# Kernel tuning notes

Hardware: AMD Instinct MI355X
Metric: run time of the kernel (lower is better)

Reference implementation:

```python
import jax, jax.numpy as jnp
import numpy as np

MODEL_DIM = 256
PAIR_IMPORTANCE_WEIGHT = 0.5
B, S, D = 4, 4096, MODEL_DIM


def setup_inputs() -> dict:
    key = jax.random.key(0)
    ks = jax.random.split(key, 6)
    return {
        "query": jax.random.normal(ks[0], (B, S, D), dtype=jnp.float32),
        "key": jax.random.normal(ks[1], (B, S, D), dtype=jnp.float32),
        "value": jax.random.normal(ks[2], (B, S, D), dtype=jnp.float32),
        "W_query": jax.random.normal(ks[3], (D, D), dtype=jnp.float32),
        "W_key": jax.random.normal(ks[4], (D, D), dtype=jnp.float32),
        "W_value": jax.random.normal(ks[5], (D, D), dtype=jnp.float32),
    }


def reference(query, key, value, W_query, W_key, W_value):
    # Projections: [B,S,D] @ [D,D]
    q = jnp.einsum('bsd,de->bse', query, W_query)
    k = jnp.einsum('bsd,de->bse', key, W_key)
    v = jnp.einsum('bsd,de->bse', value, W_value)
    scale = jnp.sqrt(jnp.asarray(MODEL_DIM, dtype=q.dtype))
    # Full [B,S,S] score matrix (global max forces materialization)
    scores = jnp.einsum('bqd,bkd->bqk', q, k) / scale
    s_len = scores.shape[1]
    diag_bias = jnp.eye(s_len, dtype=scores.dtype) * jnp.max(scores)
    scores = scores + PAIR_IMPORTANCE_WEIGHT * diag_bias  # broadcast over batch
    attention_weights = jax.nn.softmax(scores, axis=-1)
    output = jnp.einsum('bqk,bkd->bqd', attention_weights, v)
    return output, attention_weights
```

## Files before the change

### kernel.cpp

```cpp
#include <hip/hip_runtime.h>
#include <cstdint>
#include <cstddef>

#define BB 4
#define SS 4096
#define DD 256
#define SCORE_SCALE (1.0f/16.0f)
#define PIW 0.5f
#define NROWS (BB * SS)

typedef float          f32x4  __attribute__((ext_vector_type(4)));
typedef __bf16         bf16v8 __attribute__((ext_vector_type(8)));
typedef unsigned short u16v8  __attribute__((ext_vector_type(8)));
typedef unsigned short u16v4  __attribute__((ext_vector_type(4)));

__device__ __forceinline__ f32x4 mfma_bf16(u16v8 a, u16v8 b, f32x4 c) {
    return __builtin_amdgcn_mfma_f32_16x16x32_bf16(
        __builtin_bit_cast(bf16v8, a), __builtin_bit_cast(bf16v8, b), c, 0, 0, 0);
}

__device__ __forceinline__ unsigned short f2bf(float f) {
    unsigned u = __float_as_uint(f);
    u += 0x7FFFu + ((u >> 16) & 1u);
    return (unsigned short)(u >> 16);
}
__device__ __forceinline__ float bf2f(unsigned short h) {
    return __uint_as_float(((unsigned)h) << 16);
}
__device__ __forceinline__ unsigned fenc(float x) {
    unsigned u = __float_as_uint(x);
    return (u & 0x80000000u) ? ~u : (u | 0x80000000u);
}
__device__ __forceinline__ float fdec(unsigned e) {
    return __uint_as_float((e & 0x80000000u) ? (e ^ 0x80000000u) : ~e);
}

#define TM 128
#define TN 128
#define TK 16
#define PADW 132

__global__ __launch_bounds__(256) void proj_kernel(
    const float* __restrict__ query, const float* __restrict__ key_, const float* __restrict__ value,
    const float* __restrict__ Wq, const float* __restrict__ Wk, const float* __restrict__ Wv,
    unsigned short* __restrict__ qh, unsigned short* __restrict__ ql,
    unsigned short* __restrict__ kh, unsigned short* __restrict__ kl,
    unsigned short* __restrict__ vT, unsigned* __restrict__ gmax)
{
    const int z = blockIdx.z;
    const float* A = (z == 0) ? query : (z == 1) ? key_ : value;
    const float* W = (z == 0) ? Wq    : (z == 1) ? Wk   : Wv;
    if (z == 0 && blockIdx.x == 0 && blockIdx.y == 0 && threadIdx.x == 0)
        *gmax = 0x007FFFFFu;

    const int K = DD, N = DD;
    __shared__ float As[TK][PADW];
    __shared__ float Bs[TK][PADW];
    const int tid = threadIdx.x;
    const int tx = tid & 15, ty = tid >> 4;
    const int rowBase = blockIdx.y * TM;
    const int colBase = blockIdx.x * TN;

    float acc[8][8] = {};

    for (int k0 = 0; k0 < K; k0 += TK) {
        #pragma unroll
        for (int i = 0; i < 2; i++) {
            int idx = tid + i * 256;
            int r = idx >> 2, kq = idx & 3;
            const float4 av = *(const float4*)&A[(size_t)(rowBase + r) * K + k0 + kq * 4];
            As[kq * 4 + 0][r] = av.x; As[kq * 4 + 1][r] = av.y;
            As[kq * 4 + 2][r] = av.z; As[kq * 4 + 3][r] = av.w;
        }
        #pragma unroll
        for (int i = 0; i < 2; i++) {
            int idx = tid + i * 256;
            int kk = idx >> 5, cq = idx & 31;
            *(float4*)&Bs[kk][cq * 4] = *(const float4*)&W[(size_t)(k0 + kk) * N + colBase + cq * 4];
        }
        __syncthreads();
        #pragma unroll
        for (int kk = 0; kk < TK; kk++) {
            float a[8], b[8];
            *(float4*)&a[0] = *(const float4*)&As[kk][ty * 8];
            *(float4*)&a[4] = *(const float4*)&As[kk][ty * 8 + 4];
            *(float4*)&b[0] = *(const float4*)&Bs[kk][tx * 8];
            *(float4*)&b[4] = *(const float4*)&Bs[kk][tx * 8 + 4];
            #pragma unroll
            for (int i = 0; i < 8; i++)
                #pragma unroll
                for (int j = 0; j < 8; j++)
                    acc[i][j] = fmaf(a[i], b[j], acc[i][j]);
        }
        __syncthreads();
    }

    #pragma unroll
    for (int i = 0; i < 8; i++) {
        const int gr = rowBase + ty * 8 + i;
        if (z == 2) {
            const int b2 = gr >> 12, s2 = gr & (SS - 1);
            #pragma unroll
            for (int j = 0; j < 8; j++) {
                int col = colBase + tx * 8 + j;
                vT[((size_t)b2 * DD + col) * SS + s2] = f2bf(acc[i][j]);
            }
        } else {
            unsigned short h[8], l[8];
            #pragma unroll
            for (int j = 0; j < 8; j++) {
                h[j] = f2bf(acc[i][j]);
                l[j] = f2bf(acc[i][j] - bf2f(h[j]));
            }
            unsigned short* H = (z == 0) ? qh : kh;
            unsigned short* L = (z == 0) ? ql : kl;
            size_t base = (size_t)gr * DD + colBase + tx * 8;
            *(u16v4*)&H[base]     = (u16v4){h[0], h[1], h[2], h[3]};
            *(u16v4*)&H[base + 4] = (u16v4){h[4], h[5], h[6], h[7]};
            *(u16v4*)&L[base]     = (u16v4){l[0], l[1], l[2], l[3]};
            *(u16v4*)&L[base + 4] = (u16v4){l[4], l[5], l[6], l[7]};
        }
    }
}

#define SPAD 40

__global__ __launch_bounds__(256) void scores_mfma(
    const unsigned short* __restrict__ qh, const unsigned short* __restrict__ ql,
    const unsigned short* __restrict__ kh, const unsigned short* __restrict__ kl,
    float* __restrict__ attn, unsigned* __restrict__ gmax,
    float* __restrict__ tmaxg, float* __restrict__ tsumg)
{
    const int b = blockIdx.z;
    const size_t boff = (size_t)b * SS * DD;
    const unsigned short* Qh = qh + boff;
    const unsigned short* Ql = ql + boff;
    const unsigned short* Kh = kh + boff;
    const unsigned short* Kl = kl + boff;
    float* C = attn + (size_t)b * SS * SS;

    __shared__ unsigned short Ah[128][SPAD];
    __shared__ unsigned short Al[128][SPAD];
    __shared__ unsigned short Bh[128][SPAD];
    __shared__ unsigned short Bl[128][SPAD];
    __shared__ float s_m[4][64];
    __shared__ float s_s[4][64];
    __shared__ float red[128];

    const int tid = threadIdx.x;
    const int lane = tid & 63, w = tid >> 6;
    const int wr = (w >> 1) * 64, wc = (w & 1) * 64;
    const int m = lane & 15, qq = lane >> 4;
    const int rowBase = blockIdx.y * 128;
    const int colBase = blockIdx.x * 128;

    f32x4 acc[4][4];
    #pragma unroll
    for (int i = 0; i < 4; i++)
        #pragma unroll
        for (int j = 0; j < 4; j++)
            acc[i][j] = (f32x4){0.f, 0.f, 0.f, 0.f};

    const int chunk = (tid & 3) * 8;
    const int srow  = tid >> 2;

    for (int k0 = 0; k0 < DD; k0 += 32) {
        #pragma unroll
        for (int i = 0; i < 2; i++) {
            int r = srow + i * 64;
            size_t ga = (size_t)(rowBase + r) * DD + k0 + chunk;
            size_t gb = (size_t)(colBase + r) * DD + k0 + chunk;
            *(u16v8*)&Ah[r][chunk] = *(const u16v8*)&Qh[ga];
            *(u16v8*)&Al[r][chunk] = *(const u16v8*)&Ql[ga];
            *(u16v8*)&Bh[r][chunk] = *(const u16v8*)&Kh[gb];
            *(u16v8*)&Bl[r][chunk] = *(const u16v8*)&Kl[gb];
        }
        __syncthreads();

        const int kb = qq * 8;
        u16v8 ah[4], al[4], bh[4], bl[4];
        #pragma unroll
        for (int i = 0; i < 4; i++) {
            ah[i] = *(const u16v8*)&Ah[wr + i * 16 + m][kb];
            al[i] = *(const u16v8*)&Al[wr + i * 16 + m][kb];
            bh[i] = *(const u16v8*)&Bh[wc + i * 16 + m][kb];
            bl[i] = *(const u16v8*)&Bl[wc + i * 16 + m][kb];
        }
        #pragma unroll
        for (int i = 0; i < 4; i++)
            #pragma unroll
            for (int j = 0; j < 4; j++) {
                acc[i][j] = mfma_bf16(ah[i], bh[j], acc[i][j]);
                acc[i][j] = mfma_bf16(ah[i], bl[j], acc[i][j]);
                acc[i][j] = mfma_bf16(al[i], bh[j], acc[i][j]);
            }
        __syncthreads();
    }

    #pragma unroll
    for (int i = 0; i < 4; i++)
        #pragma unroll
        for (int j = 0; j < 4; j++)
            acc[i][j] *= SCORE_SCALE;

    #pragma unroll
    for (int i = 0; i < 4; i++)
        #pragma unroll
        for (int j = 0; j < 4; j++)
            #pragma unroll
            for (int r = 0; r < 4; r++) {
                int row = rowBase + wr + i * 16 + qq * 4 + r;
                int col = colBase + wc + j * 16 + m;
                __builtin_nontemporal_store(acc[i][j][r], &C[(size_t)row * SS + col]);
            }

    float lmax[16];
    #pragma unroll
    for (int i = 0; i < 4; i++)
        #pragma unroll
        for (int r = 0; r < 4; r++)
            lmax[i * 4 + r] = fmaxf(fmaxf(acc[i][0][r], acc[i][1][r]),
                                    fmaxf(acc[i][2][r], acc[i][3][r]));
    #pragma unroll
    for (int t = 0; t < 16; t++) {
        #pragma unroll
        for (int msk = 1; msk < 16; msk <<= 1)
            lmax[t] = fmaxf(lmax[t], __shfl_xor(lmax[t], msk));
    }
    if (m == 0) {
        #pragma unroll
        for (int i = 0; i < 4; i++)
            #pragma unroll
            for (int r = 0; r < 4; r++)
                s_m[w][i * 16 + qq * 4 + r] = lmax[i * 4 + r];
    }
    __syncthreads();
    float lsum[16];
    #pragma unroll
    for (int i = 0; i < 4; i++)
        #pragma unroll
        for (int r = 0; r < 4; r++) {
            int idx = i * 16 + qq * 4 + r;
            float rm = fmaxf(s_m[w][idx], s_m[w ^ 1][idx]);
            float s = 0.f;
            #pragma unroll
            for (int j = 0; j < 4; j++)
                s += __expf(acc[i][j][r] - rm);
            lsum[i * 4 + r] = s;
        }
    #pragma unroll
    for (int t = 0; t < 16; t++) {
        #pragma unroll
        for (int msk = 1; msk < 16; msk <<= 1)
            lsum[t] += __shfl_xor(lsum[t], msk);
    }
    if (m == 0) {
        #pragma unroll
        for (int i = 0; i < 4; i++)
            #pragma unroll
            for (int r = 0; r < 4; r++)
                s_s[w][i * 16 + qq * 4 + r] = lsum[i * 4 + r];
    }
    __syncthreads();

    if (tid < 128) {
        int wp = tid >> 6, lr = tid & 63;
        float tm = fmaxf(s_m[2 * wp][lr], s_m[2 * wp + 1][lr]);
        float ts = s_s[2 * wp][lr] + s_s[2 * wp + 1][lr];
        size_t gi = (size_t)blockIdx.x * NROWS + (size_t)b * SS + rowBase + tid;
        tmaxg[gi] = tm;
        tsumg[gi] = ts;
        red[tid] = tm;
    }
    __syncthreads();
    for (int s2 = 64; s2 > 0; s2 >>= 1) {
        if (tid < s2) red[tid] = fmaxf(red[tid], red[tid + s2]);
        __syncthreads();
    }
    if (tid == 0) atomicMax(gmax, fenc(red[0]));
}

__global__ __launch_bounds__(256) void stats_merge(
    const float* __restrict__ tmaxg, const float* __restrict__ tsumg,
    const float* __restrict__ attn, const unsigned* __restrict__ gmax,
    float* __restrict__ rowm, float* __restrict__ rowinv)
{
    const int grow = blockIdx.x * 256 + threadIdx.x;
    const int b = grow >> 12, i = grow & (SS - 1);
    const float bias = PIW * fdec(*gmax);

    float tm[32];
    float mx = -INFINITY;
    #pragma unroll
    for (int t = 0; t < 32; t++) {
        tm[t] = tmaxg[(size_t)t * NROWS + grow];
        mx = fmaxf(mx, tm[t]);
    }
    const float dii = attn[(size_t)b * SS * SS + (size_t)i * SS + i];
    mx = fmaxf(mx, dii + bias);

    float s = 0.f;
    #pragma unroll
    for (int t = 0; t < 32; t++)
        s += tsumg[(size_t)t * NROWS + grow] * __expf(tm[t] - mx);
    s += __expf(dii + bias - mx) - __expf(dii - mx);

    rowm[grow] = mx;
    rowinv[grow] = 1.0f / s;
}

__global__ __launch_bounds__(256) void av_softmax_mfma(
    float* __restrict__ attn, const unsigned short* __restrict__ vT,
    const float* __restrict__ rowm, const float* __restrict__ rowinv,
    const unsigned* __restrict__ gmax, float* __restrict__ out)
{
    const int lin = blockIdx.x;
    const int b = (lin & 7) >> 1;
    const int rowTile = ((lin >> 3) << 1) | (lin & 1);
    const int rowBase = rowTile * 32;

    float* A = attn + (size_t)b * SS * SS;
    const unsigned short* Bv = vT + (size_t)b * DD * SS;
    const float bias = PIW * fdec(*gmax);

    __shared__ unsigned short As[2][32][136];

    const int tid = threadIdx.x;
    const int lane = tid & 63, w = tid >> 6;
    const int m = lane & 15, qq = lane >> 4;

    const int ra = tid >> 3;
    const int c0 = (tid & 7) * 4;
    const int rr = rowBase + ra;
    float* Arow = A + (size_t)rr * SS;
    const float mr = rowm[b * SS + rr];
    const float ri = rowinv[b * SS + rr];

    const unsigned short* Bp[4];
    #pragma unroll
    for (int j = 0; j < 4; j++)
        Bp[j] = Bv + (size_t)(w * 64 + j * 16 + m) * SS;

    f32x4 acc[2][4];
    #pragma unroll
    for (int i = 0; i < 2; i++)
        #pragma unroll
        for (int j = 0; j < 4; j++)
            acc[i][j] = (f32x4){0.f, 0.f, 0.f, 0.f};

    f32x4 pf[4];

    auto loadA = [&](int kbase) {
        #pragma unroll
        for (int u = 0; u < 4; u++)
            pf[u] = __builtin_nontemporal_load(
                (const f32x4*)&Arow[kbase + c0 + u * 32]);
    };
    auto procStore = [&](int kbase, int buf) {
        #pragma unroll
        for (int u = 0; u < 4; u++) {
            int c = c0 + u * 32;
            int j0 = kbase + c;
            float e0 = pf[u][0] + ((j0 + 0 == rr) ? bias : 0.0f);
            float e1 = pf[u][1] + ((j0 + 1 == rr) ? bias : 0.0f);
            float e2 = pf[u][2] + ((j0 + 2 == rr) ? bias : 0.0f);
            float e3 = pf[u][3] + ((j0 + 3 == rr) ? bias : 0.0f);
            float w0 = __expf(e0 - mr) * ri;
            float w1 = __expf(e1 - mr) * ri;
            float w2 = __expf(e2 - mr) * ri;
            float w3 = __expf(e3 - mr) * ri;
            f32x4 wv = (f32x4){w0, w1, w2, w3};
            __builtin_nontemporal_store(wv, (f32x4*)&Arow[j0]);
            *(u16v4*)&As[buf][ra][c] =
                (u16v4){f2bf(w0), f2bf(w1), f2bf(w2), f2bf(w3)};
        }
    };

    const int NT = SS / 128;

    loadA(0);
    procStore(0, 0);
    __syncthreads();

    for (int t = 0; t < NT; t++) {
        const int k0 = t * 128;
        const int cur = t & 1;
        if (t + 1 < NT)
            loadA(k0 + 128);
        #pragma unroll
        for (int kk = 0; kk < 4; kk++) {
            const int kb = kk * 32 + qq * 8;
            u16v8 bf_[4], af_[2];
            #pragma unroll
            for (int j = 0; j < 4; j++)
                bf_[j] = *(const u16v8*)&Bp[j][k0 + kb];
            #pragma unroll
            for (int i = 0; i < 2; i++)
                af_[i] = *(const u16v8*)&As[cur][i * 16 + m][kb];
            #pragma unroll
            for (int i = 0; i < 2; i++)
                #pragma unroll
                for (int j = 0; j < 4; j++)
                    acc[i][j] = mfma_bf16(af_[i], bf_[j], acc[i][j]);
        }
        if (t + 1 < NT) {
            procStore(k0 + 128, cur ^ 1);
            __syncthreads();
        }
    }

    #pragma unroll
    for (int i = 0; i < 2; i++) {
        #pragma unroll
        for (int j = 0; j < 4; j++) {
            #pragma unroll
            for (int r = 0; r < 4; r++) {
                int row = rowBase + i * 16 + qq * 4 + r;
                int col = w * 64 + j * 16 + m;
                __builtin_nontemporal_store(
                    acc[i][j][r], &out[((size_t)b * SS + row) * DD + col]);
            }
        }
    }
}

extern "C" void kernel_launch(void* const* d_in, const int* in_sizes, int n_in,
                              void* d_out, int out_size, void* d_ws, size_t ws_size,
                              hipStream_t stream)
{
    const float* query = (const float*)d_in[0];
    const float* key_  = (const float*)d_in[1];
    const float* value = (const float*)d_in[2];
    const float* Wq    = (const float*)d_in[3];
    const float* Wk    = (const float*)d_in[4];
    const float* Wv    = (const float*)d_in[5];

    float* out  = (float*)d_out;
    float* attn = out + (size_t)BB * SS * DD;

    const size_t E = (size_t)BB * SS * DD;
    unsigned short* qh = (unsigned short*)d_ws;
    unsigned short* ql = qh + E;
    unsigned short* kh = ql + E;
    unsigned short* kl = kh + E;
    unsigned short* vT = kl + E;
    float* tmaxg  = (float*)(vT + E);
    float* tsumg  = tmaxg + 32 * (size_t)NROWS;
    float* rowm   = tsumg + 32 * (size_t)NROWS;
    float* rowinv = rowm + NROWS;
    unsigned* gmax = (unsigned*)(rowinv + NROWS);

    proj_kernel<<<dim3(DD / TN, (BB * SS) / TM, 3), 256, 0, stream>>>(
        query, key_, value, Wq, Wk, Wv, qh, ql, kh, kl, vT, gmax);
    scores_mfma<<<dim3(SS / 128, SS / 128, BB), 256, 0, stream>>>(
        qh, ql, kh, kl, attn, gmax, tmaxg, tsumg);
    stats_merge<<<dim3(NROWS / 256), 256, 0, stream>>>(
        tmaxg, tsumg, attn, gmax, rowm, rowinv);
    av_softmax_mfma<<<dim3(512), 256, 0, stream>>>(
        attn, vT, rowm, rowinv, gmax, out);
}
```

Measured before the change: 672.7 us.

## Restructure AV softmax kernel to register-resident A fragments with split-K reduction

Reworks the attention-weights-times-V kernel so each lane loads its own score fragment directly in MFMA A-operand layout, applies bias, exp and normalization in registers, and feeds it straight to the MFMA. This removes the shared-memory staging buffer and the per-tile __syncthreads. Each wave now computes all 256 output columns for 16 rows over half the key dimension. Wave pairs then combine their partial accumulators through LDS at the end. The price is a much larger register footprint (16 accumulators, 16 B fragments, two prefetch buffers), which may lower occupancy, plus more redundant V loads per wave.

```diff
diff --git a/kernel.cpp b/kernel.cpp
--- a/kernel.cpp
+++ b/kernel.cpp
@@ -309,6 +309,41 @@
     rowinv[grow] = 1.0f / s;
 }
 
+#define AV_LOADA(pf, lk)                                                      \
+    _Pragma("unroll")                                                         \
+    for (int v_ = 0; v_ < 4; v_++) {                                          \
+        pf[2*v_]   = __builtin_nontemporal_load(                              \
+            (const f32x4*)&Arow[(lk) + v_*32 + qq*8]);                        \
+        pf[2*v_+1] = __builtin_nontemporal_load(                              \
+            (const f32x4*)&Arow[(lk) + v_*32 + qq*8 + 4]);                    \
+    }
+
+#define AV_KK(pf, kkk, lk)                                                    \
+    {                                                                         \
+        const int cb_ = (lk) + (kkk)*32 + qq*8;                               \
+        _Pragma("unroll")                                                     \
+        for (int n_ = 0; n_ < 16; n_++)                                       \
+            bf[n_] = *(const u16v8*)&Bp[n_][cb_];                             \
+        f32x4 lo_ = pf[2*(kkk)], hi_ = pf[2*(kkk)+1];                         \
+        float wv_[8];                                                         \
+        _Pragma("unroll")                                                     \
+        for (int e_ = 0; e_ < 8; e_++) {                                      \
+            float x_ = (e_ < 4) ? lo_[e_ & 3] : hi_[e_ & 3];                  \
+            x_ += ((cg0 + cb_ + e_) == rr) ? bias : 0.0f;                     \
+            wv_[e_] = __expf(x_ - mr) * ri;                                   \
+        }                                                                     \
+        __builtin_nontemporal_store((f32x4){wv_[0], wv_[1], wv_[2], wv_[3]},  \
+                                    (f32x4*)&Arow[cb_]);                      \
+        __builtin_nontemporal_store((f32x4){wv_[4], wv_[5], wv_[6], wv_[7]},  \
+                                    (f32x4*)&Arow[cb_ + 4]);                  \
+        u16v8 af_ = (u16v8){f2bf(wv_[0]), f2bf(wv_[1]), f2bf(wv_[2]),         \
+                            f2bf(wv_[3]), f2bf(wv_[4]), f2bf(wv_[5]),         \
+                            f2bf(wv_[6]), f2bf(wv_[7])};                      \
+        _Pragma("unroll")                                                     \
+        for (int n_ = 0; n_ < 16; n_++)                                       \
+            acc[n_] = mfma_bf16(af_, bf[n_], acc[n_]);                        \
+    }
+
 __global__ __launch_bounds__(256) void av_softmax_mfma(
     float* __restrict__ attn, const unsigned short* __restrict__ vT,
     const float* __restrict__ rowm, const float* __restrict__ rowinv,
@@ -323,102 +358,68 @@
     const unsigned short* Bv = vT + (size_t)b * DD * SS;
     const float bias = PIW * fdec(*gmax);
 
-    __shared__ unsigned short As[2][32][136];
+    __shared__ float redl[2][64][64];
 
     const int tid = threadIdx.x;
     const int lane = tid & 63, w = tid >> 6;
+    const int pair = w >> 1;
+    const int u = w & 1;
     const int m = lane & 15, qq = lane >> 4;
 
-    const int ra = tid >> 3;
-    const int c0 = (tid & 7) * 4;
-    const int rr = rowBase + ra;
-    float* Arow = A + (size_t)rr * SS;
+    const int rr = rowBase + pair * 16 + m;
+    const int cg0 = u * 2048;
+    float* Arow = A + (size_t)rr * SS + cg0;
     const float mr = rowm[b * SS + rr];
     const float ri = rowinv[b * SS + rr];
 
-    const unsigned short* Bp[4];
-    #pragma unroll
-    for (int j = 0; j < 4; j++)
-        Bp[j] = Bv + (size_t)(w * 64 + j * 16 + m) * SS;
-
-    f32x4 acc[2][4];
-    #pragma unroll
-    for (int i = 0; i < 2; i++)
-        #pragma unroll
-        for (int j = 0; j < 4; j++)
-            acc[i][j] = (f32x4){0.f, 0.f, 0.f, 0.f};
-
-    f32x4 pf[4];
-
-    auto loadA = [&](int kbase) {
-        #pragma unroll
-        for (int u = 0; u < 4; u++)
-            pf[u] = __builtin_nontemporal_load(
-                (const f32x4*)&Arow[kbase + c0 + u * 32]);
-    };
-    auto procStore = [&](int kbase, int buf) {
-        #pragma unroll
-        for (int u = 0; u < 4; u++) {
-            int c = c0 + u * 32;
-            int j0 = kbase + c;
-            float e0 = pf[u][0] + ((j0 + 0 == rr) ? bias : 0.0f);
-            float e1 = pf[u][1] + ((j0 + 1 == rr) ? bias : 0.0f);
-            float e2 = pf[u][2] + ((j0 + 2 == rr) ? bias : 0.0f);
-            float e3 = pf[u][3] + ((j0 + 3 == rr) ? bias : 0.0f);
-            float w0 = __expf(e0 - mr) * ri;
-            float w1 = __expf(e1 - mr) * ri;
-            float w2 = __expf(e2 - mr) * ri;
-            float w3 = __expf(e3 - mr) * ri;
-            f32x4 wv = (f32x4){w0, w1, w2, w3};
-            __builtin_nontemporal_store(wv, (f32x4*)&Arow[j0]);
-            *(u16v4*)&As[buf][ra][c] =
-                (u16v4){f2bf(w0), f2bf(w1), f2bf(w2), f2bf(w3)};
-        }
-    };
-
-    const int NT = SS / 128;
-
-    loadA(0);
-    procStore(0, 0);
+    const unsigned short* Bp[16];
+    #pragma unroll
+    for (int n = 0; n < 16; n++)
+        Bp[n] = Bv + (size_t)(n * 16 + m) * SS + cg0;
+
+    f32x4 acc[16];
+    #pragma unroll
+    for (int n = 0; n < 16; n++)
+        acc[n] = (f32x4){0.f, 0.f, 0.f, 0.f};
+
+    f32x4 pfA[8], pfB[8];
+    u16v8 bf[16];
+
+    AV_LOADA(pfA, 0)
+
+    #pragma unroll 1
+    for (int t = 0; t < 16; t += 2) {
+        const int lk = t * 128;
+        AV_LOADA(pfB, lk + 128)
+        AV_KK(pfA, 0, lk)
+        AV_KK(pfA, 1, lk)
+        AV_KK(pfA, 2, lk)
+        AV_KK(pfA, 3, lk)
+        if (t + 2 < 16) {
+            AV_LOADA(pfA, lk + 256)
+        }
+        AV_KK(pfB, 0, lk + 128)
+        AV_KK(pfB, 1, lk + 128)
+        AV_KK(pfB, 2, lk + 128)
+        AV_KK(pfB, 3, lk + 128)
+    }
+
+    if (u == 1) {
+        #pragma unroll
+        for (int n = 0; n < 16; n++)
+            *(f32x4*)&redl[pair][lane][n * 4] = acc[n];
+    }
     __syncthreads();
-
-    for (int t = 0; t < NT; t++) {
-        const int k0 = t * 128;
-        const int cur = t & 1;
-        if (t + 1 < NT)
-            loadA(k0 + 128);
-        #pragma unroll
-        for (int kk = 0; kk < 4; kk++) {
-            const int kb = kk * 32 + qq * 8;
-            u16v8 bf_[4], af_[2];
-            #pragma unroll
-            for (int j = 0; j < 4; j++)
-                bf_[j] = *(const u16v8*)&Bp[j][k0 + kb];
-            #pragma unroll
-            for (int i = 0; i < 2; i++)
-                af_[i] = *(const u16v8*)&As[cur][i * 16 + m][kb];
-            #pragma unroll
-            for (int i = 0; i < 2; i++)
-                #pragma unroll
-                for (int j = 0; j < 4; j++)
-                    acc[i][j] = mfma_bf16(af_[i], bf_[j], acc[i][j]);
-        }
-        if (t + 1 < NT) {
-            procStore(k0 + 128, cur ^ 1);
-            __syncthreads();
-        }
-    }
-
-    #pragma unroll
-    for (int i = 0; i < 2; i++) {
-        #pragma unroll
-        for (int j = 0; j < 4; j++) {
+    if (u == 0) {
+        #pragma unroll
+        for (int n = 0; n < 16; n++) {
+            f32x4 o = acc[n] + *(const f32x4*)&redl[pair][lane][n * 4];
             #pragma unroll
             for (int r = 0; r < 4; r++) {
-                int row = rowBase + i * 16 + qq * 4 + r;
-                int col = w * 64 + j * 16 + m;
+                int row = rowBase + pair * 16 + qq * 4 + r;
+                int col = n * 16 + m;
                 __builtin_nontemporal_store(
-                    acc[i][j][r], &out[((size_t)b * SS + row) * DD + col]);
+                    o[r], &out[((size_t)b * SS + row) * DD + col]);
             }
         }
     }
```

New measurement: 861.4 us. 28.1% more time.
